# Kernel optimization log

Measured on AMD Instinct MI355X. Metric: run time of the kernel, lower is better.

Reference implementation:

```python
import jax, jax.numpy as jnp
import numpy as np

H, D, R, S, K, EV = 8, 256, 6, 2, 2, 2   # num_heads, head_dim, ratio, shared_head, topk, expand_v
HID = 2048
DV = D * EV            # head_v_dim = 512
KEY_DIM = H * D        # 2048
VAL_DIM = KEY_DIM * EV # 4096


def setup_inputs() -> dict:
    key = jax.random.key(0)
    ks = jax.random.split(key, 9)
    b, t = 2, 1024
    def lin(k, fan_in, shape):
        # ~torch default linear init scale
        return jax.random.normal(k, shape, jnp.float32) * (fan_in ** -0.5)
    return {
        "hidden_states": jax.random.normal(ks[0], (b, t, HID), jnp.float32),
        "Wq": lin(ks[1], HID, (HID, KEY_DIM)),
        "Wk": lin(ks[2], HID, (HID, KEY_DIM)),
        "Wv": lin(ks[3], HID, (HID, VAL_DIM)),
        "Wq_exp": lin(ks[4], D, (H, D, D * R)),  # per-head q expert expansion (ModuleList -> batched)
        "Wk_exp": lin(ks[5], D, (H, D, D * R)),
        "Wgate": lin(ks[6], D, (D, R - S)),
        "Wg": lin(ks[7], HID, (HID, VAL_DIM)),
        "Wo": lin(ks[8], VAL_DIM, (VAL_DIM, HID)),
    }


def reference(hidden_states, Wq, Wk, Wv, Wq_exp, Wk_exp, Wgate, Wg, Wo):
    b, t, _ = hidden_states.shape
    # base projections, split into heads: [H, b, t, D]
    q = (hidden_states @ Wq).reshape(b, t, H, D).transpose(2, 0, 1, 3)
    k = (hidden_states @ Wk).reshape(b, t, H, D).transpose(2, 0, 1, 3)
    v = (hidden_states @ Wv).reshape(b, t, H, DV)  # [b, t, H, DV]

    # --- sparse routing on q (gate over ratio - shared experts) ---
    logits = jnp.einsum('hbtd,dn->hbtn', q, Wgate)
    scores = jax.nn.softmax(logits.astype(jnp.float32), axis=-1)
    w, idx = jax.lax.top_k(scores, K)
    w = w / jnp.sum(w, axis=-1, keepdims=True)
    idx = idx + S  # shift past shared experts
    # scatter top-k weights into full [H, b, t, R]
    full = jnp.sum(jax.nn.one_hot(idx, R, dtype=w.dtype) * w[..., None], axis=-2)
    full = full.at[..., :S].set(1.0 / S)
    full = full / jnp.sum(full, axis=-1, keepdims=True)
    rw = full.astype(hidden_states.dtype).transpose(3, 1, 2, 0)  # [R, b, t, H]
    mask = (rw != 0).astype(hidden_states.dtype)                 # [R, b, t, H]

    # --- per-head expert expansions: [R, b, t, H, D] ---
    qe = jnp.einsum('hbtd,hde->hbte', q, Wq_exp).reshape(H, b, t, R, D).transpose(3, 1, 2, 0, 4)
    ke = jnp.einsum('hbtd,hde->hbte', k, Wk_exp).reshape(H, b, t, R, D).transpose(3, 1, 2, 0, 4)
    ve = jnp.broadcast_to(v[None], (R, b, t, H, DV))
    qe = qe * mask[..., None]
    ke = ke * mask[..., None]
    ve = ve * mask[..., None]

    # --- dense attention per (expert, batch, head) ---
    attn = jax.nn.softmax(jnp.einsum('rbqhd,rbkhd->rbhqk', qe, ke) / (D ** 0.5), axis=-1)
    o = jnp.einsum('rbhqk,rbkhd->rbqhd', attn, ve)  # [R, b, t, H, DV]

    # --- weighted combine over experts + gated output ---
    o = jnp.einsum('rbthd,rbth->bthd', o, rw)
    g = (hidden_states @ Wg).reshape(b, t, H, DV)
    o = o * jax.nn.silu(g)
    return o.reshape(b, t, VAL_DIM) @ Wo
```

## Files before the change

### kernel.cpp

```cpp
#include <hip/hip_runtime.h>
#include <hip/hip_bf16.h>
#include <cstdint>
#include <cstddef>

typedef __bf16 bf16_t;
typedef __bf16 bf16x8 __attribute__((ext_vector_type(8)));
typedef float f32x4 __attribute__((ext_vector_type(4)));

typedef __attribute__((address_space(3))) unsigned int lds_uint_t;
typedef __attribute__((address_space(1))) unsigned int glob_uint_t;

__device__ __forceinline__ void gload16(const void* g, void* l) {
  __builtin_amdgcn_global_load_lds((const glob_uint_t*)g, (lds_uint_t*)l, 16, 0, 0);
}

__device__ __forceinline__ f32x4 mfma16(bf16x8 a, bf16x8 b, f32x4 c) {
  return __builtin_amdgcn_mfma_f32_16x16x32_bf16(a, b, c, 0, 0, 0);
}

__global__ __launch_bounds__(256) void conv_bf16_k(const float* __restrict__ in,
                                                   bf16_t* __restrict__ out, int n8) {
  int i = blockIdx.x * 256 + threadIdx.x;
  if (i >= n8) return;
  f32x4 a = *(const f32x4*)(in + (size_t)i * 8);
  f32x4 b = *(const f32x4*)(in + (size_t)i * 8 + 4);
  bf16x8 o;
  o[0] = (bf16_t)a[0]; o[1] = (bf16_t)a[1]; o[2] = (bf16_t)a[2]; o[3] = (bf16_t)a[3];
  o[4] = (bf16_t)b[0]; o[5] = (bf16_t)b[1]; o[6] = (bf16_t)b[2]; o[7] = (bf16_t)b[3];
  *(bf16x8*)(out + (size_t)i * 8) = o;
}

__global__ __launch_bounds__(256) void tconv_k(const float* __restrict__ in, bf16_t* __restrict__ out,
                                               int R, int C, size_t inZ, size_t outZ) {
  __shared__ __align__(16) bf16_t t[64 * 72];
  in += (size_t)blockIdx.z * inZ;
  out += (size_t)blockIdx.z * outZ;
  const int c0 = blockIdx.x * 64, r0 = blockIdx.y * 64;
  const int tid = threadIdx.x;
#pragma unroll
  for (int it = 0; it < 4; it++) {
    int c = tid + it * 256;
    int row = c >> 4, ch = c & 15;
    f32x4 v = *(const f32x4*)(in + (size_t)(r0 + row) * C + c0 + ch * 4);
#pragma unroll
    for (int j = 0; j < 4; j++) t[(ch * 4 + j) * 72 + row] = (bf16_t)v[j];
  }
  __syncthreads();
#pragma unroll
  for (int it = 0; it < 2; it++) {
    int c = tid + it * 256;
    int oc = c >> 3, ch = c & 7;
    bf16x8 v = *(const bf16x8*)(t + oc * 72 + ch * 8);
    *(bf16x8*)(out + (size_t)(c0 + oc) * R + r0 + ch * 8) = v;
  }
}

__global__ __launch_bounds__(256) void tv_k(const bf16_t* __restrict__ v, bf16_t* __restrict__ Vt) {
  __shared__ __align__(16) bf16_t t[64 * 72];
  const int tt0 = blockIdx.x * 64;
  const int dv0 = blockIdx.y * 64;
  const int bh = blockIdx.z;
  const int b = bh >> 3, h = bh & 7;
  const int tid = threadIdx.x;
  const bf16_t* src = v + (size_t)(b * 1024 + tt0) * 4096 + h * 512 + dv0;
#pragma unroll
  for (int it = 0; it < 2; it++) {
    int c = tid + it * 256;
    int row = c >> 3, ch = c & 7;
    bf16x8 x = *(const bf16x8*)(src + (size_t)row * 4096 + ch * 8);
#pragma unroll
    for (int j = 0; j < 8; j++) t[(ch * 8 + j) * 72 + row] = x[j];
  }
  __syncthreads();
  bf16_t* dst = Vt + (size_t)bh * 524288 + (size_t)dv0 * 1024 + tt0;
#pragma unroll
  for (int it = 0; it < 2; it++) {
    int c = tid + it * 256;
    int od = c >> 3, ch = c & 7;
    bf16x8 x = *(const bf16x8*)(t + od * 72 + ch * 8);
    *(bf16x8*)(dst + (size_t)od * 1024 + ch * 8) = x;
  }
}

__global__ __launch_bounds__(256) void wfuse_k(const float* __restrict__ Wq, const float* __restrict__ Wgate,
                                               float* __restrict__ Wf) {
  __shared__ float wg[1024];
  const int tid = threadIdx.x;
  for (int i = tid; i < 1024; i += 256) wg[i] = Wgate[i];
  __syncthreads();
  const int kk = blockIdx.x * 64 + (tid & 63);
  const int oid = tid >> 6;
  float acc[8] = {0, 0, 0, 0, 0, 0, 0, 0};
  const float* wr = Wq + (size_t)kk * 2048;
#pragma unroll
  for (int half = 0; half < 2; half++) {
    const int h = oid * 2 + half;
    const float* seg = wr + h * 256;
    for (int d = 0; d < 256; d += 4) {
      f32x4 q4 = *(const f32x4*)(seg + d);
#pragma unroll
      for (int n = 0; n < 4; n++) {
        acc[half * 4 + n] += q4[0] * wg[(d + 0) * 4 + n] + q4[1] * wg[(d + 1) * 4 + n] +
                             q4[2] * wg[(d + 2) * 4 + n] + q4[3] * wg[(d + 3) * 4 + n];
      }
    }
  }
#pragma unroll
  for (int jj = 0; jj < 8; jj++) Wf[(size_t)kk * 32 + oid * 8 + jj] = acc[jj];
}

__global__ __launch_bounds__(256) void logits_k(const float* __restrict__ hs, const float* __restrict__ Wf,
                                                float* __restrict__ lg) {
  __shared__ __align__(16) float hrow[2048];
  __shared__ float red[8][32];
  const int bt = blockIdx.x;
  const int tid = threadIdx.x;
  const float* src = hs + (size_t)bt * 2048;
  for (int i = tid; i < 512; i += 256) *(f32x4*)&hrow[i * 4] = *(const f32x4*)(src + i * 4);
  __syncthreads();
  const int j = tid & 31, part = tid >> 5;
  float acc = 0.f;
  for (int kk = part * 256; kk < part * 256 + 256; kk++) acc += hrow[kk] * Wf[(size_t)kk * 32 + j];
  red[part][j] = acc;
  __syncthreads();
  if (tid < 32) {
    float s = 0.f;
#pragma unroll
    for (int p = 0; p < 8; p++) s += red[p][tid];
    lg[(size_t)bt * 32 + tid] = s;
  }
}

__global__ __launch_bounds__(256) void routing_k(const float* __restrict__ lg, float* __restrict__ rw) {
  int gid = blockIdx.x * 256 + threadIdx.x;
  if (gid >= 16384) return;
  const int h = gid >> 11;
  const int bt = gid & 2047;
  const int b = bt >> 10, tt = bt & 1023;
  f32x4 l = *(const f32x4*)(lg + (size_t)bt * 32 + h * 4);
  float mx = fmaxf(fmaxf(l[0], l[1]), fmaxf(l[2], l[3]));
  float e0 = __expf(l[0] - mx), e1 = __expf(l[1] - mx), e2 = __expf(l[2] - mx), e3 = __expf(l[3] - mx);
  float den = e0 + e1 + e2 + e3;
  float s[4] = {e0 / den, e1 / den, e2 / den, e3 / den};
  int i1 = 0;
#pragma unroll
  for (int i = 1; i < 4; i++) if (s[i] > s[i1]) i1 = i;
  int i2 = (i1 == 0) ? 1 : 0;
#pragma unroll
  for (int i = 0; i < 4; i++) if (i != i1 && s[i] > s[i2]) i2 = i;
  float sw = s[i1] + s[i2];
  float w1 = s[i1] / sw, w2 = s[i2] / sw;
  float tot = 1.0f + w1 + w2;
  float o[6] = {0.5f / tot, 0.5f / tot, 0.f, 0.f, 0.f, 0.f};
  o[2 + i1] = w1 / tot;
  o[2 + i2] = w2 / tot;
#pragma unroll
  for (int r = 0; r < 6; r++) rw[(size_t)((r * 2 + b) * 8 + h) * 1024 + tt] = o[r];
}

template <int MODE>
__global__ __launch_bounds__(256) void gemm_bt(const bf16_t* __restrict__ A, const bf16_t* __restrict__ B,
                                               void* __restrict__ Cp, int K, int lda, int ldb, int ldc,
                                               size_t aZ, size_t bZ) {
  __shared__ __align__(16) bf16_t lsA[128 * 64];
  __shared__ __align__(16) bf16_t lsB[128 * 64];
  const int tid = threadIdx.x;
  const int lane = tid & 63, wv = tid >> 6;
  const int lrow = lane & 15, lgrp = lane >> 4;
  const int wr = wv >> 1, wc = wv & 1;
  const int bn = blockIdx.x * 128, bm = blockIdx.y * 128;
  const int z = blockIdx.z;
  A += (size_t)z * aZ;
  B += (size_t)z * bZ;

  f32x4 zero = {0.f, 0.f, 0.f, 0.f};
  f32x4 acc[4][4];
#pragma unroll
  for (int i = 0; i < 4; i++)
#pragma unroll
    for (int j = 0; j < 4; j++) acc[i][j] = zero;

  for (int k0 = 0; k0 < K; k0 += 64) {
    __syncthreads();
#pragma unroll
    for (int it = 0; it < 4; it++) {
      int c = tid + it * 256;
      int row = c >> 3, coff = (c & 7) * 16;
      gload16((const char*)A + ((size_t)(bm + row) * lda + k0) * 2 + coff, (char*)lsA + row * 128 + coff);
      gload16((const char*)B + ((size_t)(bn + row) * ldb + k0) * 2 + coff, (char*)lsB + row * 128 + coff);
    }
    __syncthreads();
#pragma unroll
    for (int kk = 0; kk < 2; kk++) {
      bf16x8 af[4], bfr[4];
#pragma unroll
      for (int m4 = 0; m4 < 4; m4++)
        af[m4] = *(const bf16x8*)((const char*)lsA + (wr * 64 + m4 * 16 + lrow) * 128 + kk * 64 + lgrp * 16);
#pragma unroll
      for (int n4 = 0; n4 < 4; n4++)
        bfr[n4] = *(const bf16x8*)((const char*)lsB + (wc * 64 + n4 * 16 + lrow) * 128 + kk * 64 + lgrp * 16);
#pragma unroll
      for (int m4 = 0; m4 < 4; m4++)
#pragma unroll
        for (int n4 = 0; n4 < 4; n4++) acc[m4][n4] = mfma16(af[m4], bfr[n4], acc[m4][n4]);
    }
  }
#pragma unroll
  for (int m4 = 0; m4 < 4; m4++) {
#pragma unroll
    for (int i = 0; i < 4; i++) {
      const int row = bm + wr * 64 + m4 * 16 + lgrp * 4 + i;
#pragma unroll
      for (int n4 = 0; n4 < 4; n4++) {
        const int col = bn + wc * 64 + n4 * 16 + lrow;
        float v = acc[m4][n4][i];
        if constexpr (MODE == 0) {
          ((bf16_t*)Cp)[(size_t)row * ldc + col] = (bf16_t)v;
        } else if constexpr (MODE == 1) {
          const int bb = row >> 10, tt = row & 1023;
          const int rr = col >> 8, dd = col & 255;
          ((bf16_t*)Cp)[((size_t)((rr * 2 + bb) * 8 + z) * 1024 + tt) * 256 + dd] = (bf16_t)v;
        } else {
          ((float*)Cp)[(size_t)row * ldc + col] = v;
        }
      }
    }
  }
}

__global__ __launch_bounds__(256, 2) void attn_k(const bf16_t* __restrict__ qe, const bf16_t* __restrict__ ke,
                                                 const bf16_t* __restrict__ Vt, const float* __restrict__ rw,
                                                 const bf16_t* __restrict__ g, bf16_t* __restrict__ oc) {
  __shared__ __align__(16) bf16_t ldsK[2][32 * 256];
  __shared__ __align__(16) bf16_t ldsV[2][256 * 32];
  __shared__ __align__(16) bf16_t ldsP[4 * 16 * 40];

  const int f = (blockIdx.x & 7) * 64 + (blockIdx.x >> 3);
  const int qt = f & 15, dvh = (f >> 4) & 1, bh = f >> 5;

  const int tid = threadIdx.x;
  const int wv = tid >> 6, lane = tid & 63;
  const int lrow = lane & 15, lgrp = lane >> 4;
  const int b = bh >> 3, h = bh & 7;
  const int qw = qt * 64 + wv * 16;

  const char* vbase = (const char*)Vt + ((size_t)bh * 524288 + (size_t)dvh * 262144) * 2;

  auto issue_tile = [&](int rr, int kt, int buf) {
    const char* kb = (const char*)ke + ((size_t)((rr * 2 + b) * 8 + h) * 262144 + (size_t)kt * 8192) * 2;
    char* lk = (char*)ldsK[buf];
#pragma unroll
    for (int it = 0; it < 4; it++) {
      int p = (wv * 4 + it) * 1024 + (lane << 4);
      int row = p >> 9, off = p & 511;
      gload16(kb + (size_t)row * 512 + (off ^ ((row & 7) << 4)), lk + p);
    }
    const char* vb = vbase + kt * 64;
    char* lv = (char*)ldsV[buf];
#pragma unroll
    for (int it = 0; it < 4; it++) {
      int p = (wv * 4 + it) * 1024 + (lane << 4);
      int row = p >> 6, off = p & 63;
      gload16(vb + (size_t)row * 2048 + (off ^ (((row >> 1) & 3) << 4)), lv + p);
    }
  };

  f32x4 zero = {0.f, 0.f, 0.f, 0.f};
  f32x4 Otot[16];
#pragma unroll
  for (int n = 0; n < 16; n++) Otot[n] = zero;

  int cur = 0;
  issue_tile(0, 0, 0);

  for (int r = 0; r < 6; r++) {
    const size_t rbh = (size_t)((r * 2 + b) * 8 + h);
    const bf16_t* qbase = qe + rbh * 262144;
    const float* rwb = rw + rbh * 1024;

    bf16x8 qf[8];
#pragma unroll
    for (int c = 0; c < 8; c++)
      qf[c] = *(const bf16x8*)(qbase + (size_t)(qw + lrow) * 256 + c * 32 + lgrp * 8);
    float rwq[4];
#pragma unroll
    for (int i = 0; i < 4; i++) rwq[i] = rwb[qw + lgrp * 4 + i];

    float Lp[4] = {0.f, 0.f, 0.f, 0.f};
    f32x4 accO[16];
#pragma unroll
    for (int n = 0; n < 16; n++) accO[n] = zero;

    for (int kt = 0; kt < 32; kt++) {
      asm volatile("s_waitcnt vmcnt(0) lgkmcnt(0)" ::: "memory");
      __syncthreads();
      {
        int nr = r + ((kt == 31) ? 1 : 0);
        int nkt = (kt + 1) & 31;
        if (nr < 6) issue_tile(nr, nkt, cur ^ 1);
      }
      const char* lK = (const char*)ldsK[cur];
      const char* lV = (const char*)ldsV[cur];
      const float* rwk = rwb + kt * 32;
      float mk0 = rwk[lrow], mk1 = rwk[16 + lrow];

      f32x4 sac0 = zero, sac1 = zero;
      __builtin_amdgcn_s_setprio(1);
#pragma unroll
      for (int c = 0; c < 8; c++) {
        int col = (c * 64 + lgrp * 16) ^ ((lrow & 7) << 4);
        bf16x8 k0 = *(const bf16x8*)(lK + (size_t)lrow * 512 + col);
        bf16x8 k1 = *(const bf16x8*)(lK + (size_t)(16 + lrow) * 512 + col);
        sac0 = mfma16(qf[c], k0, sac0);
        sac1 = mfma16(qf[c], k1, sac1);
      }
      __builtin_amdgcn_s_setprio(0);
      bf16_t* pb = ldsP + wv * 640;
#pragma unroll
      for (int i = 0; i < 4; i++) {
        float e0 = __expf(sac0[i] * 0.0625f);
        float e1 = __expf(sac1[i] * 0.0625f);
        pb[(i * 4 + lgrp) * 40 + lrow] = (bf16_t)((mk0 != 0.f) ? e0 : 0.f);
        pb[(i * 4 + lgrp) * 40 + 16 + lrow] = (bf16_t)((mk1 != 0.f) ? e1 : 0.f);
        Lp[i] += ((mk0 != 0.f) ? e0 : 1.f) + ((mk1 != 0.f) ? e1 : 1.f);
      }
      bf16x8 pa = *(const bf16x8*)(pb + ((lrow & 3) * 4 + (lrow >> 2)) * 40 + lgrp * 8);
      __builtin_amdgcn_s_setprio(1);
#pragma unroll
      for (int n = 0; n < 16; n++) {
        int row = n * 16 + lrow;
        int col = (lgrp * 16) ^ (((row >> 1) & 3) << 4);
        bf16x8 vf = *(const bf16x8*)(lV + (size_t)row * 64 + col);
        accO[n] = mfma16(pa, vf, accO[n]);
      }
      __builtin_amdgcn_s_setprio(0);
      cur ^= 1;
    }
#pragma unroll
    for (int i = 0; i < 4; i++) {
      float v = Lp[i];
      v += __shfl_xor(v, 1, 16);
      v += __shfl_xor(v, 2, 16);
      v += __shfl_xor(v, 4, 16);
      v += __shfl_xor(v, 8, 16);
      float inv = rwq[i] / v;
#pragma unroll
      for (int n = 0; n < 16; n++) Otot[n][i] += accO[n][i] * inv;
    }
  }

#pragma unroll
  for (int i = 0; i < 4; i++) {
    const size_t grow = ((size_t)(b * 1024 + qw + lgrp * 4 + i)) * 8192 + h * 512 + dvh * 256;
    const size_t orow = ((size_t)(b * 1024 + qw + lgrp * 4 + i)) * 4096 + h * 512 + dvh * 256;
#pragma unroll
    for (int n = 0; n < 16; n++) {
      float gv = (float)g[grow + n * 16 + lrow];
      float sg = gv / (1.f + __expf(-gv));
      oc[orow + n * 16 + lrow] = (bf16_t)(Otot[n][i] * sg);
    }
  }
}

extern "C" void kernel_launch(void* const* d_in, const int* in_sizes, int n_in,
                              void* d_out, int out_size, void* d_ws, size_t ws_size,
                              hipStream_t stream) {
  const float* hs  = (const float*)d_in[0];
  const float* Wq  = (const float*)d_in[1];
  const float* Wk  = (const float*)d_in[2];
  const float* Wv  = (const float*)d_in[3];
  const float* Wqe = (const float*)d_in[4];
  const float* Wke = (const float*)d_in[5];
  const float* Wgt = (const float*)d_in[6];
  const float* Wg  = (const float*)d_in[7];
  const float* Wo  = (const float*)d_in[8];
  float* out = (float*)d_out;

  const size_t MB = 1024 * 1024;
  char* w = (char*)d_ws;
  bf16_t* hs_bf = (bf16_t*)(w + 0 * MB);
  bf16_t* WcatT = (bf16_t*)(w + 8 * MB);
  bf16_t* WvT   = (bf16_t*)(w + 40 * MB);
  bf16_t* qeB   = (bf16_t*)(w + 0 * MB);
  bf16_t* WoT   = (bf16_t*)(w + 56 * MB);
  bf16_t* WqeT  = (bf16_t*)(w + 72 * MB);
  bf16_t* WkeT  = (bf16_t*)(w + 78 * MB);
  bf16_t* qkg   = (bf16_t*)(w + 84 * MB);
  bf16_t* vb    = (bf16_t*)(w + 116 * MB);
  bf16_t* ocB   = (bf16_t*)(w + 116 * MB);
  bf16_t* Vt    = (bf16_t*)(w + 132 * MB);
  bf16_t* keB   = (bf16_t*)(w + 148 * MB);
  float*  Wf    = (float*)(w + 196 * MB);
  float*  lg    = (float*)(w + 196 * MB + 262144);
  float*  rwB   = (float*)(w + 196 * MB + 524288);
  (void)ws_size; (void)in_sizes; (void)n_in; (void)out_size;

  conv_bf16_k<<<2048, 256, 0, stream>>>(hs, hs_bf, 524288);
  tconv_k<<<dim3(32, 32, 1), 256, 0, stream>>>(Wq, WcatT, 2048, 2048, 0, 0);
  tconv_k<<<dim3(32, 32, 1), 256, 0, stream>>>(Wk, WcatT + 2048 * 2048, 2048, 2048, 0, 0);
  tconv_k<<<dim3(64, 32, 1), 256, 0, stream>>>(Wg, WcatT + 4096 * 2048, 2048, 4096, 0, 0);
  tconv_k<<<dim3(64, 32, 1), 256, 0, stream>>>(Wv, WvT, 2048, 4096, 0, 0);
  tconv_k<<<dim3(32, 64, 1), 256, 0, stream>>>(Wo, WoT, 4096, 2048, 0, 0);
  tconv_k<<<dim3(24, 4, 8), 256, 0, stream>>>(Wqe, WqeT, 256, 1536, 393216, 393216);
  tconv_k<<<dim3(24, 4, 8), 256, 0, stream>>>(Wke, WkeT, 256, 1536, 393216, 393216);

  wfuse_k<<<32, 256, 0, stream>>>(Wq, Wgt, Wf);
  logits_k<<<2048, 256, 0, stream>>>(hs, Wf, lg);
  routing_k<<<64, 256, 0, stream>>>(lg, rwB);

  gemm_bt<0><<<dim3(64, 16, 1), 256, 0, stream>>>(hs_bf, WcatT, qkg, 2048, 2048, 2048, 8192, 0, 0);
  gemm_bt<0><<<dim3(32, 16, 1), 256, 0, stream>>>(hs_bf, WvT, vb, 2048, 2048, 2048, 4096, 0, 0);
  tv_k<<<dim3(16, 8, 16), 256, 0, stream>>>(vb, Vt);

  gemm_bt<1><<<dim3(12, 16, 8), 256, 0, stream>>>(qkg, WqeT, qeB, 256, 8192, 256, 0, 256, 393216);
  gemm_bt<1><<<dim3(12, 16, 8), 256, 0, stream>>>(qkg + 2048, WkeT, keB, 256, 8192, 256, 0, 256, 393216);

  attn_k<<<512, 256, 0, stream>>>(qeB, keB, Vt, rwB, qkg + 4096, ocB);

  gemm_bt<2><<<dim3(16, 16, 1), 256, 0, stream>>>(ocB, WoT, out, 4096, 4096, 4096, 2048, 0, 0);
}
```

Before: 727.0 us.

## Switch attention kernel to 32x32x16 MFMA with 128-query tiles per block

The attention kernel now uses 32x32x16 bf16 MFMA instead of 16x16x32. Each wave handles 32 query rows, so each block covers 128 queries and the grid halves to 256 blocks. Every K/V tile loaded into LDS is reused by twice as many queries, which cuts LDS and global traffic per query. The P matrix layout and swizzle are rebuilt for the 32x32 fragment. The costs are larger accumulators (register pressure), the loss of the two-blocks-per-CU launch bound, and fewer blocks to spread across the CUs.

```diff
diff --git a/kernel.cpp b/kernel.cpp
--- a/kernel.cpp
+++ b/kernel.cpp
@@ -6,6 +6,7 @@
 typedef __bf16 bf16_t;
 typedef __bf16 bf16x8 __attribute__((ext_vector_type(8)));
 typedef float f32x4 __attribute__((ext_vector_type(4)));
+typedef float f32x16 __attribute__((ext_vector_type(16)));
 
 typedef __attribute__((address_space(3))) unsigned int lds_uint_t;
 typedef __attribute__((address_space(1))) unsigned int glob_uint_t;
@@ -16,6 +17,9 @@
 
 __device__ __forceinline__ f32x4 mfma16(bf16x8 a, bf16x8 b, f32x4 c) {
   return __builtin_amdgcn_mfma_f32_16x16x32_bf16(a, b, c, 0, 0, 0);
+}
+__device__ __forceinline__ f32x16 mfma32(bf16x8 a, bf16x8 b, f32x16 c) {
+  return __builtin_amdgcn_mfma_f32_32x32x16_bf16(a, b, c, 0, 0, 0);
 }
 
 __global__ __launch_bounds__(256) void conv_bf16_k(const float* __restrict__ in,
@@ -228,21 +232,21 @@
   }
 }
 
-__global__ __launch_bounds__(256, 2) void attn_k(const bf16_t* __restrict__ qe, const bf16_t* __restrict__ ke,
-                                                 const bf16_t* __restrict__ Vt, const float* __restrict__ rw,
-                                                 const bf16_t* __restrict__ g, bf16_t* __restrict__ oc) {
+__global__ __launch_bounds__(256) void attn_k(const bf16_t* __restrict__ qe, const bf16_t* __restrict__ ke,
+                                              const bf16_t* __restrict__ Vt, const float* __restrict__ rw,
+                                              const bf16_t* __restrict__ g, bf16_t* __restrict__ oc) {
   __shared__ __align__(16) bf16_t ldsK[2][32 * 256];
   __shared__ __align__(16) bf16_t ldsV[2][256 * 32];
-  __shared__ __align__(16) bf16_t ldsP[4 * 16 * 40];
-
-  const int f = (blockIdx.x & 7) * 64 + (blockIdx.x >> 3);
-  const int qt = f & 15, dvh = (f >> 4) & 1, bh = f >> 5;
+  __shared__ __align__(16) bf16_t ldsP[4][32 * 32];
+
+  const int f = (blockIdx.x & 7) * 32 + (blockIdx.x >> 3);
+  const int dvh = f & 1, qt = (f >> 1) & 7, bh = f >> 4;
 
   const int tid = threadIdx.x;
   const int wv = tid >> 6, lane = tid & 63;
-  const int lrow = lane & 15, lgrp = lane >> 4;
+  const int kq = lane & 31, hi = lane >> 5;
   const int b = bh >> 3, h = bh & 7;
-  const int qw = qt * 64 + wv * 16;
+  const int qw = qt * 128 + wv * 32;
 
   const char* vbase = (const char*)Vt + ((size_t)bh * 524288 + (size_t)dvh * 262144) * 2;
 
@@ -265,10 +269,13 @@
     }
   };
 
-  f32x4 zero = {0.f, 0.f, 0.f, 0.f};
-  f32x4 Otot[16];
-#pragma unroll
-  for (int n = 0; n < 16; n++) Otot[n] = zero;
+  f32x16 zero16 = {0.f};
+  f32x16 Otot[8];
+#pragma unroll
+  for (int n = 0; n < 8; n++) Otot[n] = zero16;
+
+  char* pw = (char*)ldsP[wv];
+  const int vr = (kq & 3) ^ ((kq >> 2) & 3);
 
   int cur = 0;
   issue_tile(0, 0, 0);
@@ -278,18 +285,19 @@
     const bf16_t* qbase = qe + rbh * 262144;
     const float* rwb = rw + rbh * 1024;
 
-    bf16x8 qf[8];
-#pragma unroll
-    for (int c = 0; c < 8; c++)
-      qf[c] = *(const bf16x8*)(qbase + (size_t)(qw + lrow) * 256 + c * 32 + lgrp * 8);
-    float rwq[4];
-#pragma unroll
-    for (int i = 0; i < 4; i++) rwq[i] = rwb[qw + lgrp * 4 + i];
-
-    float Lp[4] = {0.f, 0.f, 0.f, 0.f};
-    f32x4 accO[16];
-#pragma unroll
-    for (int n = 0; n < 16; n++) accO[n] = zero;
+    bf16x8 qf[16];
+    {
+      const bf16_t* qrow = qbase + (size_t)(qw + kq) * 256 + hi * 8;
+#pragma unroll
+      for (int s = 0; s < 16; s++) qf[s] = *(const bf16x8*)(qrow + s * 16);
+    }
+
+    float Lp[16];
+#pragma unroll
+    for (int rg = 0; rg < 16; rg++) Lp[rg] = 0.f;
+    f32x16 accO[8];
+#pragma unroll
+    for (int n = 0; n < 8; n++) accO[n] = zero16;
 
     for (int kt = 0; kt < 32; kt++) {
       asm volatile("s_waitcnt vmcnt(0) lgkmcnt(0)" ::: "memory");
@@ -301,63 +309,70 @@
       }
       const char* lK = (const char*)ldsK[cur];
       const char* lV = (const char*)ldsV[cur];
-      const float* rwk = rwb + kt * 32;
-      float mk0 = rwk[lrow], mk1 = rwk[16 + lrow];
-
-      f32x4 sac0 = zero, sac1 = zero;
+      const float mk = rwb[kt * 32 + kq];
+
+      f32x16 sA = zero16, sB = zero16;
       __builtin_amdgcn_s_setprio(1);
 #pragma unroll
-      for (int c = 0; c < 8; c++) {
-        int col = (c * 64 + lgrp * 16) ^ ((lrow & 7) << 4);
-        bf16x8 k0 = *(const bf16x8*)(lK + (size_t)lrow * 512 + col);
-        bf16x8 k1 = *(const bf16x8*)(lK + (size_t)(16 + lrow) * 512 + col);
-        sac0 = mfma16(qf[c], k0, sac0);
-        sac1 = mfma16(qf[c], k1, sac1);
+      for (int s = 0; s < 16; s += 2) {
+        bf16x8 k0 = *(const bf16x8*)(lK + (size_t)kq * 512 + ((s * 32 + hi * 16) ^ ((kq & 7) << 4)));
+        bf16x8 k1 = *(const bf16x8*)(lK + (size_t)kq * 512 + (((s + 1) * 32 + hi * 16) ^ ((kq & 7) << 4)));
+        sA = mfma32(qf[s], k0, sA);
+        sB = mfma32(qf[s + 1], k1, sB);
       }
       __builtin_amdgcn_s_setprio(0);
-      bf16_t* pb = ldsP + wv * 640;
-#pragma unroll
-      for (int i = 0; i < 4; i++) {
-        float e0 = __expf(sac0[i] * 0.0625f);
-        float e1 = __expf(sac1[i] * 0.0625f);
-        pb[(i * 4 + lgrp) * 40 + lrow] = (bf16_t)((mk0 != 0.f) ? e0 : 0.f);
-        pb[(i * 4 + lgrp) * 40 + 16 + lrow] = (bf16_t)((mk1 != 0.f) ? e1 : 0.f);
-        Lp[i] += ((mk0 != 0.f) ? e0 : 1.f) + ((mk1 != 0.f) ? e1 : 1.f);
-      }
-      bf16x8 pa = *(const bf16x8*)(pb + ((lrow & 3) * 4 + (lrow >> 2)) * 40 + lgrp * 8);
+
+      const bool act = (mk != 0.f);
+#pragma unroll
+      for (int rg = 0; rg < 16; rg++) {
+        float e = __expf((sA[rg] + sB[rg]) * 0.0625f);
+        Lp[rg] += act ? e : 1.f;
+        const int q32 = (rg & 3) + 8 * (rg >> 2) + 4 * hi;
+        const int vq = (rg & 3) ^ ((2 * (rg >> 2) + hi) & 3);
+        *(bf16_t*)(pw + q32 * 64 + ((kq * 2) ^ (vq << 4))) = (bf16_t)(act ? e : 0.f);
+      }
+
+      bf16x8 pa0 = *(const bf16x8*)(pw + kq * 64 + ((hi * 16) ^ (vr << 4)));
+      bf16x8 pa1 = *(const bf16x8*)(pw + kq * 64 + ((32 + hi * 16) ^ (vr << 4)));
       __builtin_amdgcn_s_setprio(1);
 #pragma unroll
-      for (int n = 0; n < 16; n++) {
-        int row = n * 16 + lrow;
-        int col = (lgrp * 16) ^ (((row >> 1) & 3) << 4);
-        bf16x8 vf = *(const bf16x8*)(lV + (size_t)row * 64 + col);
-        accO[n] = mfma16(pa, vf, accO[n]);
+      for (int n = 0; n < 8; n++) {
+        const size_t vrow = (size_t)(n * 32 + kq) * 64;
+        const int vswz = ((kq >> 1) & 3) << 4;
+        bf16x8 v0 = *(const bf16x8*)(lV + vrow + ((hi * 16) ^ vswz));
+        bf16x8 v1 = *(const bf16x8*)(lV + vrow + ((32 + hi * 16) ^ vswz));
+        accO[n] = mfma32(pa0, v0, accO[n]);
+        accO[n] = mfma32(pa1, v1, accO[n]);
       }
       __builtin_amdgcn_s_setprio(0);
       cur ^= 1;
     }
-#pragma unroll
-    for (int i = 0; i < 4; i++) {
-      float v = Lp[i];
-      v += __shfl_xor(v, 1, 16);
-      v += __shfl_xor(v, 2, 16);
-      v += __shfl_xor(v, 4, 16);
-      v += __shfl_xor(v, 8, 16);
-      float inv = rwq[i] / v;
-#pragma unroll
-      for (int n = 0; n < 16; n++) Otot[n][i] += accO[n][i] * inv;
-    }
-  }
-
-#pragma unroll
-  for (int i = 0; i < 4; i++) {
-    const size_t grow = ((size_t)(b * 1024 + qw + lgrp * 4 + i)) * 8192 + h * 512 + dvh * 256;
-    const size_t orow = ((size_t)(b * 1024 + qw + lgrp * 4 + i)) * 4096 + h * 512 + dvh * 256;
-#pragma unroll
-    for (int n = 0; n < 16; n++) {
-      float gv = (float)g[grow + n * 16 + lrow];
+
+#pragma unroll
+    for (int rg = 0; rg < 16; rg++) {
+      float v = Lp[rg];
+      v += __shfl_xor(v, 1, 32);
+      v += __shfl_xor(v, 2, 32);
+      v += __shfl_xor(v, 4, 32);
+      v += __shfl_xor(v, 8, 32);
+      v += __shfl_xor(v, 16, 32);
+      const int q32 = (rg & 3) + 8 * (rg >> 2) + 4 * hi;
+      float wq = rwb[qw + q32] / v;
+#pragma unroll
+      for (int n = 0; n < 8; n++) Otot[n][rg] += accO[n][rg] * wq;
+    }
+  }
+
+#pragma unroll
+  for (int rg = 0; rg < 16; rg++) {
+    const int q32 = (rg & 3) + 8 * (rg >> 2) + 4 * hi;
+    const size_t grow = ((size_t)(b * 1024 + qw + q32)) * 8192 + h * 512 + dvh * 256 + kq;
+    const size_t orow = ((size_t)(b * 1024 + qw + q32)) * 4096 + h * 512 + dvh * 256 + kq;
+#pragma unroll
+    for (int n = 0; n < 8; n++) {
+      float gv = (float)g[grow + n * 32];
       float sg = gv / (1.f + __expf(-gv));
-      oc[orow + n * 16 + lrow] = (bf16_t)(Otot[n][i] * sg);
+      oc[orow + n * 32] = (bf16_t)(Otot[n][rg] * sg);
     }
   }
 }
@@ -415,7 +430,7 @@
   gemm_bt<1><<<dim3(12, 16, 8), 256, 0, stream>>>(qkg, WqeT, qeB, 256, 8192, 256, 0, 256, 393216);
   gemm_bt<1><<<dim3(12, 16, 8), 256, 0, stream>>>(qkg + 2048, WkeT, keB, 256, 8192, 256, 0, 256, 393216);
 
-  attn_k<<<512, 256, 0, stream>>>(qeB, keB, Vt, rwB, qkg + 4096, ocB);
+  attn_k<<<256, 256, 0, stream>>>(qeB, keB, Vt, rwB, qkg + 4096, ocB);
 
   gemm_bt<2><<<dim3(16, 16, 1), 256, 0, stream>>>(ocB, WoT, out, 4096, 4096, 4096, 2048, 0, 0);
 }
```

Result: slower. 857.6 us (+18.0%).
